# Kernel optimization log

Hardware: AMD Instinct MI355X
Metric: run time of the kernel (lower is better)

Reference implementation:

```python
import jax, jax.numpy as jnp
import numpy as np

STATE_SIZE = 29
ACTION_SIZE = 3


def setup_inputs() -> dict:
    key = jax.random.key(0)
    ks = jax.random.split(key, 12)

    def row_norm(k, shape, scale=1.0):
        w = jax.random.normal(k, shape, dtype=jnp.float32)
        return w * (scale / jnp.sqrt(jnp.sum(w * w, axis=1, keepdims=True)))

    lrelu_gain = float(np.sqrt(2.0 / (1.0 + 0.01 ** 2)))  # torch calculate_gain('leaky_relu')
    inp = {
        "x": jax.random.normal(ks[0], (1, STATE_SIZE), dtype=jnp.float32),
        "hx": jnp.zeros((1, 128), jnp.float32),
        "cx": jnp.zeros((1, 128), jnp.float32),
        "w1": row_norm(ks[1], (256, STATE_SIZE)) * lrelu_gain,
        "b1": jnp.zeros((256,), jnp.float32),
        "w2": row_norm(ks[2], (256, 256)) * lrelu_gain,
        "b2": jnp.zeros((256,), jnp.float32),
        "w3": row_norm(ks[3], (128, 256)) * lrelu_gain,
        "b3": jnp.zeros((128,), jnp.float32),
        "w4": row_norm(ks[4], (128, 128)) * lrelu_gain,
        "b4": jnp.zeros((128,), jnp.float32),
        "w_ih": jax.random.normal(ks[5], (512, 128), dtype=jnp.float32) * 0.08,
        "b_ih": jnp.zeros((512,), jnp.float32),
        "w_hh": jax.random.normal(ks[6], (512, 128), dtype=jnp.float32) * 0.08,
        "b_hh": jnp.zeros((512,), jnp.float32),
        "w_critic": row_norm(ks[7], (1, 128), 1.0),
        "b_critic": jnp.zeros((1,), jnp.float32),
        "w_actor": row_norm(ks[8], (ACTION_SIZE, 128), 0.01),
        "b_actor": jnp.zeros((ACTION_SIZE,), jnp.float32),
        "w_actor2": row_norm(ks[9], (ACTION_SIZE, 128), 0.01),
        "b_actor2": jnp.zeros((ACTION_SIZE,), jnp.float32),
    }
    return inp


def _lrelu(v):
    return jnp.where(v > 0, v, 0.1 * v)


def reference(x, hx, cx, w1, b1, w2, b2, w3, b3, w4, b4,
              w_ih, b_ih, w_hh, b_hh,
              w_critic, b_critic, w_actor, b_actor, w_actor2, b_actor2):
    h = _lrelu(x @ w1.T + b1)
    h = _lrelu(h @ w2.T + b2)
    h = _lrelu(h @ w3.T + b3)
    h = _lrelu(h @ w4.T + b4)            # [1,128]
    # LSTMCell: gate order i, f, g, o (PyTorch convention)
    gates = h @ w_ih.T + b_ih + hx @ w_hh.T + b_hh  # [1,512]
    i, f, g, o = jnp.split(gates, 4, axis=-1)
    c_new = jax.nn.sigmoid(f) * cx + jax.nn.sigmoid(i) * jnp.tanh(g)
    h_new = jax.nn.sigmoid(o) * jnp.tanh(c_new)      # [1,128]
    value = jnp.squeeze(h_new @ w_critic.T + b_critic)          # scalar
    actor = jax.nn.soft_sign(h_new @ w_actor.T + b_actor)
    actor = jnp.squeeze(actor)                                   # [action_size]
    actor2 = jnp.squeeze(h_new @ w_actor2.T + b_actor2)         # [action_size]
    return (value, actor, actor2)
```

## Files before the change

kernel.cpp:

```cpp
#include <hip/hip_runtime.h>
#include <math.h>


#define NB   89
#define TPB  256
#define MAGIC 0x3A3C5A17u

#define H1_OFF 0
#define H2_OFF 256
#define H3_OFF 512
#define PT_OFF 640

__device__ __forceinline__ float lrelu(float v) { return v > 0.f ? v : 0.1f * v; }
__device__ __forceinline__ float sigm(float v)  { return 1.f / (1.f + __expf(-v)); }
__device__ __forceinline__ float dot4(float4 a, float4 b) {
    return a.x * b.x + a.y * b.y + a.z * b.z + a.w * b.w;
}

__device__ __forceinline__ void send(unsigned long long* p, float v) {
    unsigned lo = __float_as_uint(v);
    unsigned long long pk = (unsigned long long)lo |
                            ((unsigned long long)(lo ^ MAGIC) << 32);
    __hip_atomic_store(p, pk, __ATOMIC_RELAXED, __HIP_MEMORY_SCOPE_AGENT);
}
__device__ __forceinline__ float recv(unsigned long long* p) {
    unsigned long long pk =
        __hip_atomic_load(p, __ATOMIC_RELAXED, __HIP_MEMORY_SCOPE_AGENT);
    unsigned lo = (unsigned)pk, hi = (unsigned)(pk >> 32);
    if ((lo ^ MAGIC) == hi) return __uint_as_float(lo);
    __builtin_amdgcn_s_sleep(2);
    for (;;) {
        pk = __hip_atomic_load(p, __ATOMIC_RELAXED, __HIP_MEMORY_SCOPE_AGENT);
        lo = (unsigned)pk; hi = (unsigned)(pk >> 32);
        if ((lo ^ MAGIC) == hi) return __uint_as_float(lo);
        __builtin_amdgcn_s_sleep(8);
    }
}

__global__ __launch_bounds__(TPB, 1) void a3c_fwd(
    const float* __restrict__ x, const float* __restrict__ hx, const float* __restrict__ cx,
    const float* __restrict__ w1, const float* __restrict__ b1,
    const float* __restrict__ w2, const float* __restrict__ b2,
    const float* __restrict__ w3, const float* __restrict__ b3,
    const float* __restrict__ w4, const float* __restrict__ b4,
    const float* __restrict__ w_ih, const float* __restrict__ b_ih,
    const float* __restrict__ w_hh, const float* __restrict__ b_hh,
    const float* __restrict__ w_critic, const float* __restrict__ b_critic,
    const float* __restrict__ w_actor, const float* __restrict__ b_actor,
    const float* __restrict__ w_actor2, const float* __restrict__ b_actor2,
    float* __restrict__ out, unsigned long long* __restrict__ wsp)
{
    const int blk = blockIdx.x, tid = threadIdx.x;

    if (blk < 8) {
        const int row = blk * 32 + (tid >> 3), sub = tid & 7;
        float a[4];
        #pragma unroll
        for (int j = 0; j < 4; ++j) {
            int c = sub * 4 + j;
            a[j] = (c < 29) ? w1[row * 29 + c] : 0.f;
        }
        const float bb1 = b1[row];

        __shared__ __align__(16) float x_s[32];
        if (tid < 32) x_s[tid] = (tid < 29) ? x[tid] : 0.f;
        __syncthreads();

        const float* xp = x_s + sub * 4;
        float s = a[0] * xp[0] + a[1] * xp[1] + a[2] * xp[2] + a[3] * xp[3];
        s += __shfl_xor(s, 1); s += __shfl_xor(s, 2); s += __shfl_xor(s, 4);
        if (sub == 0) send(wsp + H1_OFF + row, lrelu(s + bb1));
        return;
    }

    if (blk < 40) {
        const int g  = blk - 8;
        const int gc = g * 4;
        const int r  = tid >> 4, p = tid & 15;
        const int gate = r >> 2, cell = r & 3;
        const int grow = gate * 128 + gc + cell;
        const int r4 = tid >> 1, p4 = tid & 1;

        __shared__ __align__(16) float hx_s[128];
        __shared__ __align__(16) float h3_s[128];
        __shared__ __align__(16) float h4_s[128];
        __shared__ __align__(16) float g_s[16];
        __shared__ __align__(16) float hn_s[4];
        __shared__ __align__(16) float hw_s[28];
        __shared__ __align__(16) float hb_s[8];

        float4 ah0, ah1;
        {
            const float4* wp = (const float4*)(w_hh + grow * 128 + p * 8);
            ah0 = wp[0]; ah1 = wp[1];
        }
        float4 a4[16];
        {
            const float4* wp = (const float4*)(w4 + r4 * 128 + p4 * 64);
            #pragma unroll
            for (int j = 0; j < 16; ++j) a4[j] = wp[j];
        }
        float4 ai0, ai1;
        {
            const float4* wp = (const float4*)(w_ih + grow * 128 + p * 8);
            ai0 = wp[0]; ai1 = wp[1];
        }
        const float bsum = b_ih[grow] + b_hh[grow];
        const float bb4  = b4[r4];
        float cxv = (tid < 4) ? cx[gc + tid] : 0.f;

        if (tid < 128) hx_s[tid] = hx[tid];
        if (tid < 28) {
            int o = tid >> 2, c = tid & 3;
            float v;
            if (o == 0)      v = w_critic[gc + c];
            else if (o < 4)  v = w_actor [(o - 1) * 128 + gc + c];
            else             v = w_actor2[(o - 4) * 128 + gc + c];
            hw_s[tid] = v;
        }
        if (g == 0) {
            if (tid == 224)      hb_s[0] = b_critic[0];
            else if (tid < 228 && tid > 224) hb_s[tid - 224] = b_actor[tid - 225];
            else if (tid >= 228 && tid < 231) hb_s[tid - 224] = b_actor2[tid - 228];
        }
        __syncthreads();

        float g0;
        {
            const float4* hp = (const float4*)(hx_s + p * 8);
            float s = dot4(ah0, hp[0]) + dot4(ah1, hp[1]);
            s += __shfl_xor(s, 1); s += __shfl_xor(s, 2);
            s += __shfl_xor(s, 4); s += __shfl_xor(s, 8);
            g0 = s + bsum;
        }

        if (tid < 128) h3_s[tid] = recv(wsp + H3_OFF + tid);
        __syncthreads();

        {
            const float4* hp = (const float4*)(h3_s + p4 * 64);
            float s = 0.f;
            #pragma unroll
            for (int j = 0; j < 16; ++j) s += dot4(a4[j], hp[j]);
            s += __shfl_xor(s, 1);
            if (p4 == 0) h4_s[r4] = lrelu(s + bb4);
        }
        __syncthreads();

        {
            const float4* hp = (const float4*)(h4_s + p * 8);
            float s = dot4(ai0, hp[0]) + dot4(ai1, hp[1]);
            s += __shfl_xor(s, 1); s += __shfl_xor(s, 2);
            s += __shfl_xor(s, 4); s += __shfl_xor(s, 8);
            if (p == 0) g_s[r] = g0 + s;
        }
        __syncthreads();

        if (tid < 4) {
            float ig = g_s[tid];
            float fg = g_s[4 + tid];
            float gg = g_s[8 + tid];
            float og = g_s[12 + tid];
            float c  = sigm(fg) * cxv + sigm(ig) * tanhf(gg);
            hn_s[tid] = sigm(og) * tanhf(c);
        }
        __syncthreads();

        if (tid < 7) {
            const float* wc = hw_s + tid * 4;
            float s = wc[0] * hn_s[0] + wc[1] * hn_s[1]
                    + wc[2] * hn_s[2] + wc[3] * hn_s[3];
            if (g == 0) s += hb_s[tid];
            send(wsp + PT_OFF + tid * 32 + g, s);
        }
        return;
    }

    if (blk < 72) {
        const int row = (blk - 40) * 8 + (tid >> 5), p = tid & 31;
        float4 a0, a1v;
        {
            const float4* wp = (const float4*)(w2 + row * 256 + p * 8);
            a0 = wp[0]; a1v = wp[1];
        }
        const float bb2 = b2[row];

        __shared__ __align__(16) float h1_s[256];
        h1_s[tid] = recv(wsp + H1_OFF + tid);
        __syncthreads();

        const float4* hp = (const float4*)(h1_s + p * 8);
        float s = dot4(a0, hp[0]) + dot4(a1v, hp[1]);
        s += __shfl_xor(s, 1); s += __shfl_xor(s, 2);
        s += __shfl_xor(s, 4); s += __shfl_xor(s, 8);
        s += __shfl_xor(s, 16);
        if (p == 0) send(wsp + H2_OFF + row, lrelu(s + bb2));
        return;
    }

    if (blk < 88) {
        const int row = (blk - 72) * 8 + (tid >> 5), p = tid & 31;
        float4 a0, a1v;
        {
            const float4* wp = (const float4*)(w3 + row * 256 + p * 8);
            a0 = wp[0]; a1v = wp[1];
        }
        const float bb3 = b3[row];

        __shared__ __align__(16) float h2_s[256];
        h2_s[tid] = recv(wsp + H2_OFF + tid);
        __syncthreads();

        const float4* hp = (const float4*)(h2_s + p * 8);
        float s = dot4(a0, hp[0]) + dot4(a1v, hp[1]);
        s += __shfl_xor(s, 1); s += __shfl_xor(s, 2);
        s += __shfl_xor(s, 4); s += __shfl_xor(s, 8);
        s += __shfl_xor(s, 16);
        if (p == 0) send(wsp + H3_OFF + row, lrelu(s + bb3));
        return;
    }

    if (tid < 224) {
        float s = recv(wsp + PT_OFF + tid);
        const int o = tid >> 5, k = tid & 31;
        s += __shfl_xor(s, 1); s += __shfl_xor(s, 2);
        s += __shfl_xor(s, 4); s += __shfl_xor(s, 8);
        s += __shfl_xor(s, 16);
        if (k == 0) {
            float r = s;
            if (o >= 1 && o <= 3) r = r / (1.f + fabsf(r));
            out[o] = r;
        }
    }
}

extern "C" void kernel_launch(void* const* d_in, const int* in_sizes, int n_in,
                              void* d_out, int out_size, void* d_ws, size_t ws_size,
                              hipStream_t stream) {
    const float* x        = (const float*)d_in[0];
    const float* hx       = (const float*)d_in[1];
    const float* cx       = (const float*)d_in[2];
    const float* w1       = (const float*)d_in[3];
    const float* b1       = (const float*)d_in[4];
    const float* w2       = (const float*)d_in[5];
    const float* b2       = (const float*)d_in[6];
    const float* w3       = (const float*)d_in[7];
    const float* b3       = (const float*)d_in[8];
    const float* w4       = (const float*)d_in[9];
    const float* b4       = (const float*)d_in[10];
    const float* w_ih     = (const float*)d_in[11];
    const float* b_ih     = (const float*)d_in[12];
    const float* w_hh     = (const float*)d_in[13];
    const float* b_hh     = (const float*)d_in[14];
    const float* w_critic = (const float*)d_in[15];
    const float* b_critic = (const float*)d_in[16];
    const float* w_actor  = (const float*)d_in[17];
    const float* b_actor  = (const float*)d_in[18];
    const float* w_actor2 = (const float*)d_in[19];
    const float* b_actor2 = (const float*)d_in[20];
    float* out = (float*)d_out;
    unsigned long long* wsp = (unsigned long long*)d_ws;

    a3c_fwd<<<NB, TPB, 0, stream>>>(x, hx, cx, w1, b1, w2, b2, w3, b3, w4, b4,
                                    w_ih, b_ih, w_hh, b_hh,
                                    w_critic, b_critic, w_actor, b_actor,
                                    w_actor2, b_actor2, out, wsp);
}
```

Before: 102.1 us.

## Consolidate dataflow blocks, prefetch mailbox lines, and repack partial-sum layout

Cuts the grid from 89 to 61 blocks by giving each block more rows: layer 1 uses 4 blocks of 64 rows, layers 2 and 3 use 16 and 8 blocks of 16 rows, and the LSTM blocks get the lowest block indices. Each block issues early atomic loads ('touch') on the mailbox cache lines it will later poll or write, to warm them before the spin-wait. The partial-sum mailbox is relaid out so each LSTM block writes 8 contiguous slots, and the final block gathers them through shared memory with a serial sum. The goals are fewer blocks to schedule, lower first-poll latency, and fewer cache lines touched per block. In exchange, each thread now does more work per row, and the final reduction is serial.

```diff
diff --git a/kernel.cpp b/kernel.cpp
--- a/kernel.cpp
+++ b/kernel.cpp
@@ -2,7 +2,7 @@
 #include <math.h>
 
 
-#define NB   89
+#define NB   61
 #define TPB  256
 #define MAGIC 0x3A3C5A17u
 
@@ -35,6 +35,11 @@
         if ((lo ^ MAGIC) == hi) return __uint_as_float(lo);
         __builtin_amdgcn_s_sleep(8);
     }
+}
+__device__ __forceinline__ void touch(unsigned long long* p) {
+    unsigned long long v =
+        __hip_atomic_load(p, __ATOMIC_RELAXED, __HIP_MEMORY_SCOPE_AGENT);
+    asm volatile("" :: "v"(v));
 }
 
 __global__ __launch_bounds__(TPB, 1) void a3c_fwd(
@@ -52,34 +57,16 @@
 {
     const int blk = blockIdx.x, tid = threadIdx.x;
 
-    if (blk < 8) {
-        const int row = blk * 32 + (tid >> 3), sub = tid & 7;
-        float a[4];
-        #pragma unroll
-        for (int j = 0; j < 4; ++j) {
-            int c = sub * 4 + j;
-            a[j] = (c < 29) ? w1[row * 29 + c] : 0.f;
-        }
-        const float bb1 = b1[row];
-
-        __shared__ __align__(16) float x_s[32];
-        if (tid < 32) x_s[tid] = (tid < 29) ? x[tid] : 0.f;
-        __syncthreads();
-
-        const float* xp = x_s + sub * 4;
-        float s = a[0] * xp[0] + a[1] * xp[1] + a[2] * xp[2] + a[3] * xp[3];
-        s += __shfl_xor(s, 1); s += __shfl_xor(s, 2); s += __shfl_xor(s, 4);
-        if (sub == 0) send(wsp + H1_OFF + row, lrelu(s + bb1));
-        return;
-    }
-
-    if (blk < 40) {
-        const int g  = blk - 8;
+    if (blk < 32) {
+        const int g  = blk;
         const int gc = g * 4;
         const int r  = tid >> 4, p = tid & 15;
         const int gate = r >> 2, cell = r & 3;
         const int grow = gate * 128 + gc + cell;
         const int r4 = tid >> 1, p4 = tid & 1;
+
+        if (tid < 8)       touch(wsp + H3_OFF + tid * 16);
+        else if (tid == 8) touch(wsp + PT_OFF + g * 8);
 
         __shared__ __align__(16) float hx_s[128];
         __shared__ __align__(16) float h3_s[128];
@@ -118,10 +105,10 @@
             else             v = w_actor2[(o - 4) * 128 + gc + c];
             hw_s[tid] = v;
         }
-        if (g == 0) {
-            if (tid == 224)      hb_s[0] = b_critic[0];
-            else if (tid < 228 && tid > 224) hb_s[tid - 224] = b_actor[tid - 225];
-            else if (tid >= 228 && tid < 231) hb_s[tid - 224] = b_actor2[tid - 228];
+        if (g == 0 && tid == 0) {
+            hb_s[0] = b_critic[0];
+            hb_s[1] = b_actor[0];  hb_s[2] = b_actor[1];  hb_s[3] = b_actor[2];
+            hb_s[4] = b_actor2[0]; hb_s[5] = b_actor2[1]; hb_s[6] = b_actor2[2];
         }
         __syncthreads();
 
@@ -171,17 +158,47 @@
             float s = wc[0] * hn_s[0] + wc[1] * hn_s[1]
                     + wc[2] * hn_s[2] + wc[3] * hn_s[3];
             if (g == 0) s += hb_s[tid];
-            send(wsp + PT_OFF + tid * 32 + g, s);
-        }
-        return;
-    }
-
-    if (blk < 72) {
-        const int row = (blk - 40) * 8 + (tid >> 5), p = tid & 31;
-        float4 a0, a1v;
-        {
-            const float4* wp = (const float4*)(w2 + row * 256 + p * 8);
-            a0 = wp[0]; a1v = wp[1];
+            send(wsp + PT_OFF + g * 8 + tid, s);
+        }
+        return;
+    }
+
+    if (blk < 36) {
+        const int row = (blk - 32) * 64 + (tid >> 2), sub = tid & 3;
+        if (tid < 4) touch(wsp + H1_OFF + (blk - 32) * 64 + tid * 16);
+
+        float a[8];
+        #pragma unroll
+        for (int j = 0; j < 8; ++j) {
+            int c = sub * 8 + j;
+            a[j] = (c < 29) ? w1[row * 29 + c] : 0.f;
+        }
+        const float bb1 = b1[row];
+
+        __shared__ __align__(16) float x_s[32];
+        if (tid < 32) x_s[tid] = (tid < 29) ? x[tid] : 0.f;
+        __syncthreads();
+
+        const float* xp = x_s + sub * 8;
+        float s = 0.f;
+        #pragma unroll
+        for (int j = 0; j < 8; ++j) s += a[j] * xp[j];
+        s += __shfl_xor(s, 1); s += __shfl_xor(s, 2);
+        if (sub == 0) send(wsp + H1_OFF + row, lrelu(s + bb1));
+        return;
+    }
+
+    if (blk < 52) {
+        const int b = blk - 36;
+        const int row = b * 16 + (tid >> 4), p = tid & 15;
+        if (tid < 16)       touch(wsp + H1_OFF + tid * 16);
+        else if (tid == 16) touch(wsp + H2_OFF + b * 16);
+
+        float4 a2[4];
+        {
+            const float4* wp = (const float4*)(w2 + row * 256 + p * 16);
+            #pragma unroll
+            for (int j = 0; j < 4; ++j) a2[j] = wp[j];
         }
         const float bb2 = b2[row];
 
@@ -189,21 +206,27 @@
         h1_s[tid] = recv(wsp + H1_OFF + tid);
         __syncthreads();
 
-        const float4* hp = (const float4*)(h1_s + p * 8);
-        float s = dot4(a0, hp[0]) + dot4(a1v, hp[1]);
+        const float4* hp = (const float4*)(h1_s + p * 16);
+        float s = 0.f;
+        #pragma unroll
+        for (int j = 0; j < 4; ++j) s += dot4(a2[j], hp[j]);
         s += __shfl_xor(s, 1); s += __shfl_xor(s, 2);
         s += __shfl_xor(s, 4); s += __shfl_xor(s, 8);
-        s += __shfl_xor(s, 16);
         if (p == 0) send(wsp + H2_OFF + row, lrelu(s + bb2));
         return;
     }
 
-    if (blk < 88) {
-        const int row = (blk - 72) * 8 + (tid >> 5), p = tid & 31;
-        float4 a0, a1v;
-        {
-            const float4* wp = (const float4*)(w3 + row * 256 + p * 8);
-            a0 = wp[0]; a1v = wp[1];
+    if (blk < 60) {
+        const int b = blk - 52;
+        const int row = b * 16 + (tid >> 4), p = tid & 15;
+        if (tid < 16)       touch(wsp + H2_OFF + tid * 16);
+        else if (tid == 16) touch(wsp + H3_OFF + b * 16);
+
+        float4 a3[4];
+        {
+            const float4* wp = (const float4*)(w3 + row * 256 + p * 16);
+            #pragma unroll
+            for (int j = 0; j < 4; ++j) a3[j] = wp[j];
         }
         const float bb3 = b3[row];
 
@@ -211,25 +234,29 @@
         h2_s[tid] = recv(wsp + H2_OFF + tid);
         __syncthreads();
 
-        const float4* hp = (const float4*)(h2_s + p * 8);
-        float s = dot4(a0, hp[0]) + dot4(a1v, hp[1]);
+        const float4* hp = (const float4*)(h2_s + p * 16);
+        float s = 0.f;
+        #pragma unroll
+        for (int j = 0; j < 4; ++j) s += dot4(a3[j], hp[j]);
         s += __shfl_xor(s, 1); s += __shfl_xor(s, 2);
         s += __shfl_xor(s, 4); s += __shfl_xor(s, 8);
-        s += __shfl_xor(s, 16);
         if (p == 0) send(wsp + H3_OFF + row, lrelu(s + bb3));
         return;
     }
 
-    if (tid < 224) {
-        float s = recv(wsp + PT_OFF + tid);
-        const int o = tid >> 5, k = tid & 31;
-        s += __shfl_xor(s, 1); s += __shfl_xor(s, 2);
-        s += __shfl_xor(s, 4); s += __shfl_xor(s, 8);
-        s += __shfl_xor(s, 16);
-        if (k == 0) {
-            float r = s;
-            if (o >= 1 && o <= 3) r = r / (1.f + fabsf(r));
-            out[o] = r;
+    {
+        if (tid < 32) touch(wsp + PT_OFF + tid * 8);
+        __shared__ __align__(16) float ps[224];
+        const int g = tid >> 3, h = tid & 7;
+        if (h < 7) ps[h * 32 + g] = recv(wsp + PT_OFF + g * 8 + h);
+        __syncthreads();
+        if (tid < 7) {
+            const float* row = ps + tid * 32;
+            float s = 0.f;
+            #pragma unroll
+            for (int j = 0; j < 32; ++j) s += row[j];
+            if (tid >= 1 && tid <= 3) s = s / (1.f + fabsf(s));
+            out[tid] = s;
         }
     }
 }
```

Result: no change. 103.0 us (+0.9%).
